# Performance work log

Hardware: AMD Instinct MI355X
Metric: run time of the kernel (lower is better)

Reference implementation:

```python
import jax, jax.numpy as jnp
import numpy as np

N_NODES = 50000
N_EDGES = 600000
D = 128
APPNP_K = 5
APPNP_ALPHA = 0.2


def _mish(x):
    return x * jnp.tanh(jax.nn.softplus(x))


def setup_inputs() -> dict:
    key = jax.random.key(0)
    ks = jax.random.split(key, 6)
    x = jax.random.normal(ks[0], (N_NODES, D), dtype=jnp.float32)
    src = jax.random.randint(ks[1], (N_EDGES,), 0, N_NODES, dtype=jnp.int32)
    dst = jax.random.randint(ks[2], (N_EDGES,), 0, N_NODES, dtype=jnp.int32)
    W1 = jax.random.normal(ks[3], (D, D), dtype=jnp.float32) * (1.0 / np.sqrt(D))
    b1 = jnp.zeros((D,), dtype=jnp.float32)
    W2 = jax.random.normal(ks[4], (2 * D, D), dtype=jnp.float32) * (1.0 / np.sqrt(2 * D))
    b2 = jnp.zeros((D,), dtype=jnp.float32)
    eps1 = jnp.zeros((1,), dtype=jnp.float32)
    eps2 = jnp.zeros((1,), dtype=jnp.float32)
    return {"x": x, "src": src, "dst": dst, "W1": W1, "b1": b1,
            "W2": W2, "b2": b2, "eps1": eps1, "eps2": eps2}


def _appnp(x0, src, dst):
    # DGL APPNPConv: symmetric degree normalization, k power-iteration steps.
    ones = jnp.ones((src.shape[0],), dtype=x0.dtype)
    deg_out = jnp.clip(jax.ops.segment_sum(ones, src, num_segments=N_NODES), 1.0)
    deg_in = jnp.clip(jax.ops.segment_sum(ones, dst, num_segments=N_NODES), 1.0)
    norm_o = deg_out[:, None] ** -0.5  # [N,1]
    norm_i = deg_in[:, None] ** -0.5
    h = x0
    for _ in range(APPNP_K):
        h = h * norm_o
        h = jax.ops.segment_sum(h[src], dst, num_segments=N_NODES)  # gather-scatter
        h = h * norm_i
        h = (1.0 - APPNP_ALPHA) * h + APPNP_ALPHA * x0
    return h


def _gin(h, src, dst, eps, W, b):
    # GINConv(sum, learn_eps): (1+eps)*h + sum_{j in N(i)} h_j, then Linear.
    agg = jax.ops.segment_sum(h[src], dst, num_segments=N_NODES)
    return ((1.0 + eps) * h + agg) @ W + b


def reference(x, src, dst, W1, b1, W2, b2, eps1, eps2):
    out = jnp.tanh(x)           # GCNNorm affects edge weights only; node feats then tanh
    x0 = out                    # res_out[0]
    out = _appnp(out, src, dst)
    out = _gin(out, src, dst, eps1[0], W1, b1)          # layer 0
    out = jnp.concatenate([out, x0], axis=1)            # residual concat
    out = _gin(out, src, dst, eps2[0], W2, b2)          # layer 1
    return _mish(out)
```

## Files before the change

kernel.cpp:

```cpp
#include <hip/hip_runtime.h>
#include <hip/hip_fp16.h>
#include <math.h>

#define NN 50000
#define NE 600000
#define NT ((NN + 31) / 32)

#define HB 64
#define HBINS 12500

typedef _Float16 half8_t __attribute__((ext_vector_type(8)));
typedef float f32x16 __attribute__((ext_vector_type(16)));
typedef float f32x2 __attribute__((ext_vector_type(2)));

union F2H { float2 f; __half2 h[2]; };

__device__ __forceinline__ float2 fp8_dec(unsigned short u) {
  f32x2 v = __builtin_amdgcn_cvt_pk_f32_fp8((unsigned int)u, false);
  float2 r; r.x = v.x; r.y = v.y; return r;
}
__device__ __forceinline__ unsigned short fp8_enc(float a, float b) {
  return (unsigned short)__builtin_amdgcn_cvt_pk_fp8_f32(a, b, 0u, false);
}


__global__ __launch_bounds__(256) void k_tanh(const float* __restrict__ x,
                                              const float* __restrict__ no,
                                              __half2* __restrict__ x0h,
                                              unsigned int* __restrict__ x0n8) {
  int i = blockIdx.x * 256 + threadIdx.x;
  if (i >= NN * 32) return;
  float4 v = reinterpret_cast<const float4*>(x)[i];
  float t[4];
  float vv[4] = {v.x, v.y, v.z, v.w};
  #pragma unroll
  for (int j = 0; j < 4; ++j) {
    float xc = fminf(fmaxf(vv[j], -9.f), 9.f);
    float E = __expf(2.f * xc);
    t[j] = (E - 1.f) / (E + 1.f);
  }
  float s = no[i >> 5];
  F2H a;
  a.h[0] = __floats2half2_rn(t[0], t[1]);
  a.h[1] = __floats2half2_rn(t[2], t[3]);
  reinterpret_cast<float2*>(x0h)[i] = a.f;
  unsigned int p = __builtin_amdgcn_cvt_pk_fp8_f32(t[0] * s, t[1] * s, 0u, false);
  p = __builtin_amdgcn_cvt_pk_fp8_f32(t[2] * s, t[3] * s, p, true);
  x0n8[i] = p;
}

__global__ __launch_bounds__(256) void k_wt(const float* __restrict__ W1,
                                            const float* __restrict__ W2,
                                            _Float16* __restrict__ w1p,
                                            _Float16* __restrict__ w2p) {
  int i = blockIdx.x * 256 + threadIdx.x;
  if (i < 128 * 128) {
    int k = i >> 7, n = i & 127;
    int nb = n >> 5, r = n & 31, ks = k >> 4, g = (k & 15) >> 3, j = k & 7;
    w1p[(((ks << 2) + nb) * 64 + (g << 5) + r) * 8 + j] = (_Float16)W1[i];
  } else {
    int q = i - 128 * 128;
    if (q < 256 * 128) {
      int k = q >> 7, n = q & 127;
      int nb = n >> 5, r = n & 31, ks = k >> 4, g = (k & 15) >> 3, j = k & 7;
      w2p[(((ks << 2) + nb) * 64 + (g << 5) + r) * 8 + j] = (_Float16)W2[q];
    }
  }
}

__global__ __launch_bounds__(1024) void k_hist(const int* __restrict__ src,
                                               const int* __restrict__ dst,
                                               int* __restrict__ hpart) {
  __shared__ int lh[HBINS];
  #pragma unroll 1
  for (int ph = 0; ph < 8; ++ph) {
    const int* idx = (ph & 4) ? dst : src;
    int base = (ph & 3) * HBINS;
    for (int i = threadIdx.x; i < HBINS; i += 1024) lh[i] = 0;
    __syncthreads();
    for (int e = blockIdx.x * 1024 + threadIdx.x; e < NE; e += HB * 1024) {
      int v = idx[e] - base;
      if ((unsigned)v < (unsigned)HBINS) atomicAdd(&lh[v], 1);
    }
    __syncthreads();
    int* outp = hpart + ((size_t)ph * HB + blockIdx.x) * HBINS;
    for (int i = threadIdx.x; i < HBINS; i += 1024) outp[i] = lh[i];
    __syncthreads();
  }
}

__global__ __launch_bounds__(256) void k_merge(const int* __restrict__ hpart,
                                               int* __restrict__ ci,
                                               float* __restrict__ no,
                                               float* __restrict__ ni) {
  int i = blockIdx.x * 256 + threadIdx.x;
  if (i >= NN) return;
  int r = i / HBINS, bin = i - r * HBINS;
  const int* ps = hpart + ((size_t)(0 + r) * HB) * HBINS + bin;
  const int* pd = hpart + ((size_t)(4 + r) * HB) * HBINS + bin;
  int so = 0, si = 0;
  #pragma unroll 8
  for (int b = 0; b < HB; ++b) {
    so += ps[(size_t)b * HBINS];
    si += pd[(size_t)b * HBINS];
  }
  ci[i] = si;
  no[i] = rsqrtf((float)max(so, 1));
  ni[i] = rsqrtf((float)max(si, 1));
}

__global__ __launch_bounds__(1024) void k_scanA(const int* __restrict__ deg,
                                                int* __restrict__ incl,
                                                int* __restrict__ bsum) {
  int tid = threadIdx.x;
  int gid = blockIdx.x * 1024 + tid;
  int v = (gid < NN) ? deg[gid] : 0;
  int lane = tid & 63;
  #pragma unroll
  for (int o = 1; o < 64; o <<= 1) {
    int n = __shfl_up(v, o);
    if (lane >= o) v += n;
  }
  __shared__ int ws[16];
  int wid = tid >> 6;
  if (lane == 63) ws[wid] = v;
  __syncthreads();
  if (tid < 16) {
    int s = ws[tid];
    #pragma unroll
    for (int o = 1; o < 16; o <<= 1) {
      int n = __shfl_up(s, o);
      if (tid >= o) s += n;
    }
    ws[tid] = s;
  }
  __syncthreads();
  if (wid > 0) v += ws[wid - 1];
  if (gid < NN) incl[gid] = v;
  if (tid == 1023) bsum[blockIdx.x] = v;
}

__global__ __launch_bounds__(64) void k_scanB(const int* __restrict__ bsum,
                                              int* __restrict__ boff, int nb) {
  int t = threadIdx.x;
  int v = (t < nb) ? bsum[t] : 0;
  int orig = v;
  #pragma unroll
  for (int o = 1; o < 64; o <<= 1) {
    int n = __shfl_up(v, o);
    if (t >= o) v += n;
  }
  if (t < nb) boff[t] = v - orig;
}

__global__ __launch_bounds__(256) void k_scanC(const int* __restrict__ incl,
                                               const int* __restrict__ deg,
                                               const int* __restrict__ boff,
                                               int* __restrict__ rp) {
  int i = blockIdx.x * 256 + threadIdx.x;
  if (i < NN) rp[i] = incl[i] - deg[i] + boff[i >> 10];
  if (i == 0) rp[NN] = NE;
}

__global__ __launch_bounds__(256) void k_fill(const int* __restrict__ src,
                                              const int* __restrict__ dst,
                                              const int* __restrict__ rp,
                                              int* __restrict__ fill,
                                              int* __restrict__ colsrc) {
  int e = blockIdx.x * 256 + threadIdx.x;
  if (e < NE) {
    int d = dst[e];
    int pos = rp[d] + atomicAdd(&fill[d], 1);
    colsrc[pos] = src[e];
  }
}

#define GATHER_LOOP(LOADEXPR)                                        \
  for (int base = 0; base < cnt; base += 64) {                      \
    int e = beg + base + lane;                                      \
    int cv = (e < end) ? cs[e] : 0;                                 \
    int m = cnt - base; if (m > 64) m = 64;                         \
    int j = 0;                                                      \
    for (; j + 8 <= m; j += 8) {                                    \
      _Pragma("unroll")                                             \
      for (int u = 0; u < 8; ++u) {                                 \
        int s = __builtin_amdgcn_readlane(cv, j + u);               \
        LOADEXPR;                                                   \
      }                                                             \
    }                                                               \
    for (; j < m; ++j) {                                            \
      int s = __builtin_amdgcn_readlane(cv, j);                     \
      LOADEXPR;                                                     \
    }                                                               \
  }

template <bool LAST>
__global__ __launch_bounds__(256) void k_appnp8(const unsigned short* __restrict__ h8,
                                                const __half2* __restrict__ x0,
                                                const float* __restrict__ no,
                                                const float* __restrict__ ni,
                                                const int* __restrict__ rp,
                                                const int* __restrict__ cs,
                                                unsigned short* __restrict__ out8,
                                                __half2* __restrict__ out16) {
  int w = (blockIdx.x * 256 + threadIdx.x) >> 6;
  int lane = threadIdx.x & 63;
  if (w >= NN) return;
  const unsigned short* hl = h8 + lane;
  int beg = rp[w], end = rp[w + 1], cnt = end - beg;
  float ax = 0.f, ay = 0.f;
  GATHER_LOOP({
    float2 f = fp8_dec(hl[s * 64]);
    ax += f.x; ay += f.y;
  })
  float wi = 0.8f * ni[w];
  float2 xv = __half22float2(x0[w * 64 + lane]);
  float rx = wi * ax + 0.2f * xv.x;
  float ry = wi * ay + 0.2f * xv.y;
  if (LAST) {
    out16[w * 64 + lane] = __floats2half2_rn(rx, ry);
  } else {
    float sc = no[w];
    out8[w * 64 + lane] = fp8_enc(rx * sc, ry * sc);
  }
}

__device__ inline void store_packed(_Float16* __restrict__ zp, int w, int lane,
                                    float v0, float v1) {
  int t = w >> 5, r = w & 31;
  int ks = lane >> 3, g = (lane >> 2) & 1, j = (lane & 3) * 2;
  size_t addr = (((size_t)t * 8 + ks) * 64 + g * 32 + r) * 8 + j;
  *reinterpret_cast<__half2*>(zp + addr) = __floats2half2_rn(v0, v1);
}

__global__ __launch_bounds__(256) void k_appnp_first(const unsigned short* __restrict__ xs8,
                                                     const __half2* __restrict__ xp,
                                                     const float* __restrict__ epsp,
                                                     const float* __restrict__ no,
                                                     const float* __restrict__ ni,
                                                     const int* __restrict__ rp,
                                                     const int* __restrict__ cs,
                                                     unsigned short* __restrict__ hout8,
                                                     _Float16* __restrict__ zout) {
  int w = (blockIdx.x * 256 + threadIdx.x) >> 6;
  int lane = threadIdx.x & 63;
  if (w >= NN) return;
  const unsigned short* xsl = xs8 + lane;
  const __half2* xpl = xp + lane;
  int beg = rp[w], end = rp[w + 1], cnt = end - beg;
  float ax = 0.f, ay = 0.f, bx = 0.f, by = 0.f;
  GATHER_LOOP({
    float2 f = fp8_dec(xsl[s * 64]);
    float2 g2 = __half22float2(xpl[s * 64]);
    ax += f.x; ay += f.y; bx += g2.x; by += g2.y;
  })
  float2 xv = __half22float2(xp[w * 64 + lane]);
  float wi = 0.8f * ni[w];
  float sc = no[w];
  hout8[w * 64 + lane] = fp8_enc(sc * (wi * ax + 0.2f * xv.x),
                                 sc * (wi * ay + 0.2f * xv.y));
  float e2 = 1.0f + epsp[0];
  store_packed(zout, w, lane, e2 * xv.x + bx, e2 * xv.y + by);
}

__global__ __launch_bounds__(256) void k_gather_z(const __half2* __restrict__ h,
                                                  const float* __restrict__ epsp,
                                                  const int* __restrict__ rp,
                                                  const int* __restrict__ cs,
                                                  _Float16* __restrict__ zout) {
  int w = (blockIdx.x * 256 + threadIdx.x) >> 6;
  int lane = threadIdx.x & 63;
  if (w >= NN) return;
  const __half2* hl = h + lane;
  int beg = rp[w], end = rp[w + 1], cnt = end - beg;
  float ax = 0.f, ay = 0.f;
  GATHER_LOOP({
    float2 f = __half22float2(hl[s * 64]);
    ax += f.x; ay += f.y;
  })
  float e1 = 1.0f + epsp[0];
  float2 hv = __half22float2(h[w * 64 + lane]);
  store_packed(zout, w, lane, e1 * hv.x + ax, e1 * hv.y + ay);
}

template <int KTOT, bool MISH>
__global__ __launch_bounds__(64) void k_mgemm(const _Float16* __restrict__ z0,
                                              const _Float16* __restrict__ z1,
                                              const _Float16* __restrict__ wp,
                                              const float* __restrict__ bias,
                                              float* __restrict__ outf,
                                              __half2* __restrict__ outh) {
  int lane = threadIdx.x;
  int t = blockIdx.x;
  int row0 = t * 32;
  if (row0 >= NN) return;
  int r31 = lane & 31, g = lane >> 5;
  f32x16 acc[4];
  #pragma unroll
  for (int i = 0; i < 4; ++i) acc[i] = (f32x16)(0.0f);
  #pragma unroll 4
  for (int ks = 0; ks < KTOT / 16; ++ks) {
    const _Float16* zp = (KTOT == 256 && ks >= 8) ? z1 : z0;
    int kls = (KTOT == 256) ? (ks & 7) : ks;
    half8_t a = *reinterpret_cast<const half8_t*>(
        zp + (((size_t)t * 8 + kls) * 64 + lane) * 8);
    #pragma unroll
    for (int nb = 0; nb < 4; ++nb) {
      half8_t b = *reinterpret_cast<const half8_t*>(
          wp + (((size_t)ks * 4 + nb) * 64 + lane) * 8);
      acc[nb] = __builtin_amdgcn_mfma_f32_32x32x16_f16(a, b, acc[nb], 0, 0, 0);
    }
  }
  #pragma unroll
  for (int nb = 0; nb < 4; ++nb) {
    float bv = bias[nb * 32 + r31];
    #pragma unroll
    for (int r = 0; r < 16; ++r) {
      int rl = (r & 3) + 8 * (r >> 2) + 4 * g;
      int grow = row0 + rl;
      if (grow < NN) {
        float v = acc[nb][r] + bv;
        if (MISH) {
          float E = __expf(v);
          float q = E * (E + 2.f);
          float mv = v * q / (q + 2.f);
          v = (v > 15.f) ? v : mv;
          outf[(size_t)grow * 128 + nb * 32 + r31] = v;
        } else {
          float u = __shfl_xor(v, 1);
          if (!(lane & 1)) {
            outh[((size_t)grow * 128 + nb * 32 + r31) >> 1] = __floats2half2_rn(v, u);
          }
        }
      }
    }
  }
}

extern "C" void kernel_launch(void* const* d_in, const int* in_sizes, int n_in,
                              void* d_out, int out_size, void* d_ws, size_t ws_size,
                              hipStream_t stream) {
  const float* x = (const float*)d_in[0];
  const int* src = (const int*)d_in[1];
  const int* dst = (const int*)d_in[2];
  const float* W1 = (const float*)d_in[3];
  const float* b1 = (const float*)d_in[4];
  const float* W2 = (const float*)d_in[5];
  const float* b2 = (const float*)d_in[6];
  const float* eps1 = (const float*)d_in[7];
  const float* eps2 = (const float*)d_in[8];
  float* out = (float*)d_out;

  char* ws = (char*)d_ws;
  size_t off = 0;
  auto alloc = [&](size_t bytes) -> void* {
    void* p = ws + off;
    off += (bytes + 255) & ~(size_t)255;
    return p;
  };
  const size_t NDP = (size_t)NT * 4096;
  __half2* x0h = (__half2*)alloc(NDP * 2);
  unsigned short* x0n8 = (unsigned short*)alloc(NDP);
  unsigned short* hA8 = (unsigned short*)alloc(NDP);
  unsigned short* hB8 = (unsigned short*)alloc(NDP);
  __half2* h5 = (__half2*)alloc(NDP * 2);
  __half2* zx = (__half2*)alloc(NDP * 2);
  __half2* z1p = (__half2*)alloc(NDP * 2);
  __half2* g1h = (__half2*)alloc(NDP * 2);
  __half2* zg = (__half2*)alloc(NDP * 2);
  _Float16* w1p = (_Float16*)alloc(128 * 128 * 2);
  _Float16* w2p = (_Float16*)alloc(256 * 128 * 2);
  int* ci = (int*)alloc(NN * 4);
  int* fillc = (int*)alloc(NN * 4);
  float* nrm_o = (float*)alloc(NN * 4);
  float* nrm_i = (float*)alloc(NN * 4);
  int* incl = (int*)alloc(NN * 4);
  int* bsum = (int*)alloc(64 * 4);
  int* boff = (int*)alloc(64 * 4);
  int* rp = (int*)alloc((NN + 1) * 4);
  int* colsrc = (int*)alloc(NE * 4);

  int* hpart = (int*)zx;

  hipMemsetAsync(fillc, 0, NN * 4, stream);

  k_hist<<<HB, 1024, 0, stream>>>(src, dst, hpart);
  k_merge<<<(NN + 255) / 256, 256, 0, stream>>>(hpart, ci, nrm_o, nrm_i);

  const int SB = (NN + 1023) / 1024;
  k_scanA<<<SB, 1024, 0, stream>>>(ci, incl, bsum);
  k_scanB<<<1, 64, 0, stream>>>(bsum, boff, SB);
  k_scanC<<<(NN + 255) / 256, 256, 0, stream>>>(incl, ci, boff, rp);
  const int EB = (NE + 255) / 256;
  k_fill<<<EB, 256, 0, stream>>>(src, dst, rp, fillc, colsrc);

  k_tanh<<<(NN * 32 + 255) / 256, 256, 0, stream>>>(x, nrm_o, x0h,
                                                    (unsigned int*)x0n8);
  k_wt<<<192, 256, 0, stream>>>(W1, W2, w1p, w2p);

  const int GB = (NN * 64 + 255) / 256;
  k_appnp_first<<<GB, 256, 0, stream>>>(x0n8, x0h, eps2, nrm_o, nrm_i, rp, colsrc,
                                        hA8, (_Float16*)zx);
  k_appnp8<false><<<GB, 256, 0, stream>>>(hA8, x0h, nrm_o, nrm_i, rp, colsrc,
                                          hB8, nullptr);
  k_appnp8<false><<<GB, 256, 0, stream>>>(hB8, x0h, nrm_o, nrm_i, rp, colsrc,
                                          hA8, nullptr);
  k_appnp8<false><<<GB, 256, 0, stream>>>(hA8, x0h, nrm_o, nrm_i, rp, colsrc,
                                          hB8, nullptr);
  k_appnp8<true><<<GB, 256, 0, stream>>>(hB8, x0h, nrm_o, nrm_i, rp, colsrc,
                                         nullptr, h5);

  k_gather_z<<<GB, 256, 0, stream>>>(h5, eps1, rp, colsrc, (_Float16*)z1p);

  k_mgemm<128, false><<<NT, 64, 0, stream>>>((const _Float16*)z1p, nullptr, w1p, b1,
                                             nullptr, g1h);
  k_gather_z<<<GB, 256, 0, stream>>>(g1h, eps2, rp, colsrc, (_Float16*)zg);
  k_mgemm<256, true><<<NT, 64, 0, stream>>>((const _Float16*)zg, (const _Float16*)zx,
                                            w2p, b2, out, nullptr);
}
```

Before: 332.7 us.

## Split APPNP gather into feature-half blocks, replace atomic CSR fill with per-range LDS placement

APPNP propagation now processes each node in two half-feature blocks, one byte per lane, arranged so that neighbouring blocks share the same feature half. The aim is to shrink the working set each gather touches and improve L2 locality. The fused first APPNP step that also produced the GIN z-input is split back into a plain APPNP step plus a separate gather_z pass over x0. The CSR fill switches from global atomics to 64 blocks that each scan all edges and count their own dst range with LDS atomics, which avoids the memset but makes every block read the full edge list.

```diff
diff --git a/kernel.cpp b/kernel.cpp
--- a/kernel.cpp
+++ b/kernel.cpp
@@ -8,6 +8,8 @@
 
 #define HB 64
 #define HBINS 12500
+#define PB 64
+#define PRANGE ((NN + PB - 1) / PB)
 
 typedef _Float16 half8_t __attribute__((ext_vector_type(8)));
 typedef float f32x16 __attribute__((ext_vector_type(16)));
@@ -15,12 +17,12 @@
 
 union F2H { float2 f; __half2 h[2]; };
 
-__device__ __forceinline__ float2 fp8_dec(unsigned short u) {
-  f32x2 v = __builtin_amdgcn_cvt_pk_f32_fp8((unsigned int)u, false);
-  float2 r; r.x = v.x; r.y = v.y; return r;
-}
-__device__ __forceinline__ unsigned short fp8_enc(float a, float b) {
-  return (unsigned short)__builtin_amdgcn_cvt_pk_fp8_f32(a, b, 0u, false);
+__device__ __forceinline__ float fp8_dec1(unsigned int u) {
+  f32x2 v = __builtin_amdgcn_cvt_pk_f32_fp8(u, false);
+  return v.x;
+}
+__device__ __forceinline__ unsigned char fp8_enc1(float a) {
+  return (unsigned char)__builtin_amdgcn_cvt_pk_fp8_f32(a, a, 0u, false);
 }
 
 
@@ -162,16 +164,21 @@
   if (i == 0) rp[NN] = NE;
 }
 
-__global__ __launch_bounds__(256) void k_fill(const int* __restrict__ src,
-                                              const int* __restrict__ dst,
-                                              const int* __restrict__ rp,
-                                              int* __restrict__ fill,
-                                              int* __restrict__ colsrc) {
-  int e = blockIdx.x * 256 + threadIdx.x;
-  if (e < NE) {
-    int d = dst[e];
-    int pos = rp[d] + atomicAdd(&fill[d], 1);
-    colsrc[pos] = src[e];
+__global__ __launch_bounds__(1024) void k_place(const int* __restrict__ src,
+                                                const int* __restrict__ dst,
+                                                const int* __restrict__ rp,
+                                                int* __restrict__ colsrc) {
+  __shared__ int lc[PRANGE];
+  int base = blockIdx.x * PRANGE;
+  int lim = NN - base; if (lim > PRANGE) lim = PRANGE;
+  for (int i = threadIdx.x; i < PRANGE; i += 1024) lc[i] = 0;
+  __syncthreads();
+  for (int e = threadIdx.x; e < NE; e += 1024) {
+    int d = dst[e] - base;
+    if ((unsigned)d < (unsigned)lim) {
+      int pos = rp[base + d] + atomicAdd(&lc[d], 1);
+      colsrc[pos] = src[e];
+    }
   }
 }
 
@@ -195,33 +202,34 @@
   }
 
 template <bool LAST>
-__global__ __launch_bounds__(256) void k_appnp8(const unsigned short* __restrict__ h8,
-                                                const __half2* __restrict__ x0,
-                                                const float* __restrict__ no,
-                                                const float* __restrict__ ni,
-                                                const int* __restrict__ rp,
-                                                const int* __restrict__ cs,
-                                                unsigned short* __restrict__ out8,
-                                                __half2* __restrict__ out16) {
-  int w = (blockIdx.x * 256 + threadIdx.x) >> 6;
+__global__ __launch_bounds__(256) void k_appnp8s(const unsigned char* __restrict__ h8,
+                                                 const __half* __restrict__ x0,
+                                                 const float* __restrict__ no,
+                                                 const float* __restrict__ ni,
+                                                 const int* __restrict__ rp,
+                                                 const int* __restrict__ cs,
+                                                 unsigned char* __restrict__ out8,
+                                                 __half* __restrict__ out16) {
+  int bid = blockIdx.x;
+  int hf = (bid >> 2) & 1;
+  int grp = (bid >> 3) * 4 + (bid & 3);
+  int w = grp * 4 + (threadIdx.x >> 6);
   int lane = threadIdx.x & 63;
   if (w >= NN) return;
-  const unsigned short* hl = h8 + lane;
+  const unsigned char* hl = h8 + hf * 64 + lane;
   int beg = rp[w], end = rp[w + 1], cnt = end - beg;
-  float ax = 0.f, ay = 0.f;
+  float a = 0.f;
   GATHER_LOOP({
-    float2 f = fp8_dec(hl[s * 64]);
-    ax += f.x; ay += f.y;
+    unsigned int uv = hl[(size_t)s * 128];
+    a += fp8_dec1(uv);
   })
   float wi = 0.8f * ni[w];
-  float2 xv = __half22float2(x0[w * 64 + lane]);
-  float rx = wi * ax + 0.2f * xv.x;
-  float ry = wi * ay + 0.2f * xv.y;
+  float xv = __half2float(x0[(size_t)w * 128 + hf * 64 + lane]);
+  float r = wi * a + 0.2f * xv;
   if (LAST) {
-    out16[w * 64 + lane] = __floats2half2_rn(rx, ry);
+    out16[(size_t)w * 128 + hf * 64 + lane] = __float2half(r);
   } else {
-    float sc = no[w];
-    out8[w * 64 + lane] = fp8_enc(rx * sc, ry * sc);
+    out8[(size_t)w * 128 + hf * 64 + lane] = fp8_enc1(r * no[w]);
   }
 }
 
@@ -231,36 +239,6 @@
   int ks = lane >> 3, g = (lane >> 2) & 1, j = (lane & 3) * 2;
   size_t addr = (((size_t)t * 8 + ks) * 64 + g * 32 + r) * 8 + j;
   *reinterpret_cast<__half2*>(zp + addr) = __floats2half2_rn(v0, v1);
-}
-
-__global__ __launch_bounds__(256) void k_appnp_first(const unsigned short* __restrict__ xs8,
-                                                     const __half2* __restrict__ xp,
-                                                     const float* __restrict__ epsp,
-                                                     const float* __restrict__ no,
-                                                     const float* __restrict__ ni,
-                                                     const int* __restrict__ rp,
-                                                     const int* __restrict__ cs,
-                                                     unsigned short* __restrict__ hout8,
-                                                     _Float16* __restrict__ zout) {
-  int w = (blockIdx.x * 256 + threadIdx.x) >> 6;
-  int lane = threadIdx.x & 63;
-  if (w >= NN) return;
-  const unsigned short* xsl = xs8 + lane;
-  const __half2* xpl = xp + lane;
-  int beg = rp[w], end = rp[w + 1], cnt = end - beg;
-  float ax = 0.f, ay = 0.f, bx = 0.f, by = 0.f;
-  GATHER_LOOP({
-    float2 f = fp8_dec(xsl[s * 64]);
-    float2 g2 = __half22float2(xpl[s * 64]);
-    ax += f.x; ay += f.y; bx += g2.x; by += g2.y;
-  })
-  float2 xv = __half22float2(xp[w * 64 + lane]);
-  float wi = 0.8f * ni[w];
-  float sc = no[w];
-  hout8[w * 64 + lane] = fp8_enc(sc * (wi * ax + 0.2f * xv.x),
-                                 sc * (wi * ay + 0.2f * xv.y));
-  float e2 = 1.0f + epsp[0];
-  store_packed(zout, w, lane, e2 * xv.x + bx, e2 * xv.y + by);
 }
 
 __global__ __launch_bounds__(256) void k_gather_z(const __half2* __restrict__ h,
@@ -360,9 +338,9 @@
   };
   const size_t NDP = (size_t)NT * 4096;
   __half2* x0h = (__half2*)alloc(NDP * 2);
-  unsigned short* x0n8 = (unsigned short*)alloc(NDP);
-  unsigned short* hA8 = (unsigned short*)alloc(NDP);
-  unsigned short* hB8 = (unsigned short*)alloc(NDP);
+  unsigned char* x0n8 = (unsigned char*)alloc(NDP);
+  unsigned char* hA8 = (unsigned char*)alloc(NDP);
+  unsigned char* hB8 = (unsigned char*)alloc(NDP);
   __half2* h5 = (__half2*)alloc(NDP * 2);
   __half2* zx = (__half2*)alloc(NDP * 2);
   __half2* z1p = (__half2*)alloc(NDP * 2);
@@ -371,7 +349,6 @@
   _Float16* w1p = (_Float16*)alloc(128 * 128 * 2);
   _Float16* w2p = (_Float16*)alloc(256 * 128 * 2);
   int* ci = (int*)alloc(NN * 4);
-  int* fillc = (int*)alloc(NN * 4);
   float* nrm_o = (float*)alloc(NN * 4);
   float* nrm_i = (float*)alloc(NN * 4);
   int* incl = (int*)alloc(NN * 4);
@@ -382,8 +359,6 @@
 
   int* hpart = (int*)zx;
 
-  hipMemsetAsync(fillc, 0, NN * 4, stream);
-
   k_hist<<<HB, 1024, 0, stream>>>(src, dst, hpart);
   k_merge<<<(NN + 255) / 256, 256, 0, stream>>>(hpart, ci, nrm_o, nrm_i);
 
@@ -391,25 +366,27 @@
   k_scanA<<<SB, 1024, 0, stream>>>(ci, incl, bsum);
   k_scanB<<<1, 64, 0, stream>>>(bsum, boff, SB);
   k_scanC<<<(NN + 255) / 256, 256, 0, stream>>>(incl, ci, boff, rp);
-  const int EB = (NE + 255) / 256;
-  k_fill<<<EB, 256, 0, stream>>>(src, dst, rp, fillc, colsrc);
+  k_place<<<PB, 1024, 0, stream>>>(src, dst, rp, colsrc);
 
   k_tanh<<<(NN * 32 + 255) / 256, 256, 0, stream>>>(x, nrm_o, x0h,
                                                     (unsigned int*)x0n8);
   k_wt<<<192, 256, 0, stream>>>(W1, W2, w1p, w2p);
 
+  const __half* x0hs = (const __half*)x0h;
+  const int AB = 25000;
+  k_appnp8s<false><<<AB, 256, 0, stream>>>(x0n8, x0hs, nrm_o, nrm_i, rp, colsrc,
+                                           hA8, nullptr);
+  k_appnp8s<false><<<AB, 256, 0, stream>>>(hA8, x0hs, nrm_o, nrm_i, rp, colsrc,
+                                           hB8, nullptr);
+  k_appnp8s<false><<<AB, 256, 0, stream>>>(hB8, x0hs, nrm_o, nrm_i, rp, colsrc,
+                                           hA8, nullptr);
+  k_appnp8s<false><<<AB, 256, 0, stream>>>(hA8, x0hs, nrm_o, nrm_i, rp, colsrc,
+                                           hB8, nullptr);
+  k_appnp8s<true><<<AB, 256, 0, stream>>>(hB8, x0hs, nrm_o, nrm_i, rp, colsrc,
+                                          nullptr, (__half*)h5);
+
   const int GB = (NN * 64 + 255) / 256;
-  k_appnp_first<<<GB, 256, 0, stream>>>(x0n8, x0h, eps2, nrm_o, nrm_i, rp, colsrc,
-                                        hA8, (_Float16*)zx);
-  k_appnp8<false><<<GB, 256, 0, stream>>>(hA8, x0h, nrm_o, nrm_i, rp, colsrc,
-                                          hB8, nullptr);
-  k_appnp8<false><<<GB, 256, 0, stream>>>(hB8, x0h, nrm_o, nrm_i, rp, colsrc,
-                                          hA8, nullptr);
-  k_appnp8<false><<<GB, 256, 0, stream>>>(hA8, x0h, nrm_o, nrm_i, rp, colsrc,
-                                          hB8, nullptr);
-  k_appnp8<true><<<GB, 256, 0, stream>>>(hB8, x0h, nrm_o, nrm_i, rp, colsrc,
-                                         nullptr, h5);
-
+  k_gather_z<<<GB, 256, 0, stream>>>(x0h, eps2, rp, colsrc, (_Float16*)zx);
   k_gather_z<<<GB, 256, 0, stream>>>(h5, eps1, rp, colsrc, (_Float16*)z1p);
 
   k_mgemm<128, false><<<NT, 64, 0, stream>>>((const _Float16*)z1p, nullptr, w1p, b1,
```

After: 685.9 us. 106% more time.
